# Kernel tuning notes

Measured on AMD Instinct MI355X. Metric: run time of the kernel, lower is better.

The kernel has to match this reference:

```python
import jax, jax.numpy as jnp
import numpy as np

N_NODES = 1_000_000
N_EDGES = 32_000_000

def setup_inputs() -> dict:
    key = jax.random.key(0)
    ks = jax.random.split(key, 7)
    x = jax.random.normal(ks[0], (N_NODES, 1), dtype=jnp.float32)
    edge_index = jax.random.randint(ks[1], (2, N_EDGES), 0, N_NODES, dtype=jnp.int32)
    W1 = jax.random.normal(ks[2], (1, 4), dtype=jnp.float32)
    b1 = jax.random.normal(ks[3], (4,), dtype=jnp.float32)
    W2 = jax.random.normal(ks[4], (4, 1), dtype=jnp.float32)
    b2 = jax.random.normal(ks[5], (1,), dtype=jnp.float32)
    Wsage = jax.random.normal(ks[6], (1, 1), dtype=jnp.float32)
    return {"x": x, "edge_index": edge_index, "W1": W1, "b1": b1,
            "W2": W2, "b2": b2, "Wsage": Wsage}

def reference(x, edge_index, W1, b1, W2, b2, Wsage):
    # MLP: Linear(1,4) -> ReLU -> Linear(4,1)
    h = jax.nn.relu(x @ W1 + b1) @ W2 + b2  # [N,1]
    # SAGEConv(1,1, root_weight=False, bias=False): mean-aggregate neighbors, then linear
    src, dst = edge_index[0], edge_index[1]
    n = h.shape[0]
    msgs = jnp.take(h, src, axis=0)                       # [E,1] gather
    summed = jax.ops.segment_sum(msgs, dst, num_segments=n)  # [N,1]
    cnt = jax.ops.segment_sum(jnp.ones((msgs.shape[0], 1), h.dtype), dst, num_segments=n)
    mean = summed / jnp.maximum(cnt, 1.0)                 # isolated nodes -> 0
    return mean @ Wsage
```

## Files before the change

kernel.cpp:

```cpp
#include <hip/hip_runtime.h>

__global__ void node_mlp_kernel(const float* __restrict__ x,
                                const float* __restrict__ W1,
                                const float* __restrict__ b1,
                                const float* __restrict__ W2,
                                const float* __restrict__ b2,
                                float* __restrict__ h, int N) {
    const float w10 = W1[0], w11 = W1[1], w12 = W1[2], w13 = W1[3];
    const float b10 = b1[0], b11 = b1[1], b12 = b1[2], b13 = b1[3];
    const float w20 = W2[0], w21 = W2[1], w22 = W2[2], w23 = W2[3];
    const float b2v = b2[0];
    int i = blockIdx.x * blockDim.x + threadIdx.x;
    if (i < N) {
        float xv = x[i];
        float acc = b2v;
        acc += fmaxf(fmaf(xv, w10, b10), 0.0f) * w20;
        acc += fmaxf(fmaf(xv, w11, b11), 0.0f) * w21;
        acc += fmaxf(fmaf(xv, w12, b12), 0.0f) * w22;
        acc += fmaxf(fmaf(xv, w13, b13), 0.0f) * w23;
        h[i] = acc;
    }
}

#define NBINS    256
#define NSUB     8
#define BIN_CAP  131072
#define SUBCAP   (BIN_CAP / NSUB)
#define CHUNK    4096
#define BLK      256
#define EPT      16
#define MAGIC_SH 42
#define PBITS    12
#define VBITS    17
#define VBIAS    (1 << (VBITS - 1))
#define VMAX     (VBIAS - 1)

__global__ void init_cursor_kernel(int* __restrict__ cursor) {
    int t = blockIdx.x * blockDim.x + threadIdx.x;
    if (t < NBINS * NSUB) cursor[t] = (t >> 3) * BIN_CAP + (t & (NSUB - 1)) * SUBCAP;
}

__device__ __forceinline__ int bin_of(int d, unsigned long long magic) {
    return (int)(((unsigned long long)(unsigned)d * magic) >> MAGIC_SH);
}

__global__ __launch_bounds__(BLK, 4)
void bin_scatter_kernel(const int* __restrict__ src,
                        const int* __restrict__ dst,
                        const float* __restrict__ h,
                        int* __restrict__ cursor,
                        unsigned* __restrict__ binned, int E,
                        int DIV, unsigned long long magic) {
    __shared__ int  lhist[NBINS];
    __shared__ int  lbase[NBINS];
    __shared__ int  gbase[NBINS];
    __shared__ int2 stage[CHUNK];

    const int t = threadIdx.x;
    lhist[t] = 0;
    __syncthreads();

    const int e0 = blockIdx.x * CHUNK;
    const int e1 = min(E, e0 + CHUNK);
    const int nval = e1 - e0;
    const int k = blockIdx.x & (NSUB - 1);

    int pk[EPT];
    int rk[EPT];
    #pragma unroll
    for (int it = 0; it < EPT / 4; ++it) {
        int e = e0 + 4 * (t + it * BLK);
        int4 d;
        if (e + 3 < e1) {
            d = *(const int4*)(dst + e);
        } else {
            d.x = (e + 0 < e1) ? dst[e + 0] : -1;
            d.y = (e + 1 < e1) ? dst[e + 1] : -1;
            d.z = (e + 2 < e1) ? dst[e + 2] : -1;
            d.w = (e + 3 < e1) ? dst[e + 3] : -1;
        }
        #pragma unroll
        for (int j = 0; j < 4; ++j) {
            int dd = (j == 0) ? d.x : (j == 1) ? d.y : (j == 2) ? d.z : d.w;
            int p = -1, r = 0;
            if (dd >= 0) {
                int b = bin_of(dd, magic);
                p = (b << PBITS) | (dd - b * DIV);
                r = atomicAdd(&lhist[b], 1);
            }
            pk[4 * it + j] = p;
            rk[4 * it + j] = r;
        }
    }
    __syncthreads();

    if (t < 64) {
        const int b4 = t * 4;
        int v[4]; int s = 0;
        #pragma unroll
        for (int j = 0; j < 4; ++j) { v[j] = lhist[b4 + j]; s += v[j]; }
        int inc = s;
        #pragma unroll
        for (int dlt = 1; dlt < 64; dlt <<= 1) {
            int u = __shfl_up(inc, dlt, 64);
            if (t >= dlt) inc += u;
        }
        int excl = inc - s;
        #pragma unroll
        for (int j = 0; j < 4; ++j) {
            lbase[b4 + j] = excl; excl += v[j];
        }
    }
    __syncthreads();

    int r0 = atomicAdd(&cursor[t * NSUB + k], lhist[t]);

    #pragma unroll
    for (int it = 0; it < EPT / 4; ++it) {
        int e = e0 + 4 * (t + it * BLK);
        int4 s4 = make_int4(0, 0, 0, 0);
        if (e + 3 < e1) {
            s4 = *(const int4*)(src + e);
        } else {
            if (e + 0 < e1) s4.x = src[e + 0];
            if (e + 1 < e1) s4.y = src[e + 1];
            if (e + 2 < e1) s4.z = src[e + 2];
            if (e + 3 < e1) s4.w = src[e + 3];
        }
        #pragma unroll
        for (int j = 0; j < 4; ++j) {
            int p = pk[4 * it + j];
            if (p >= 0) {
                int ss = (j == 0) ? s4.x : (j == 1) ? s4.y : (j == 2) ? s4.z : s4.w;
                int fx = __float2int_rn(h[ss] * 256.0f);
                fx = min(max(fx, -VMAX), VMAX) + VBIAS;
                int slot = lbase[p >> PBITS] + rk[4 * it + j];
                stage[slot] = make_int2(p, fx);
            }
        }
    }
    gbase[t] = r0;
    __syncthreads();

    const int subend_off = (k + 1) * SUBCAP;
    for (int i = t; i < nval; i += BLK) {
        int2 ent = stage[i];
        int b = ent.x >> PBITS;
        int addr = gbase[b] + (i - lbase[b]);
        if (addr < b * BIN_CAP + subend_off)
            binned[addr] = ((unsigned)(ent.x & ((1 << PBITS) - 1)) << VBITS)
                           | (unsigned)ent.y;
    }
}

#define RBLK 1024

__global__ __launch_bounds__(RBLK)
void bin_reduce_kernel(const unsigned* __restrict__ binned,
                       const int* __restrict__ cursor,
                       const float* __restrict__ Wsage,
                       float* __restrict__ out, int N, int DIV) {
    extern __shared__ unsigned acc32[];
    const int b = blockIdx.x;
    const int t = threadIdx.x;
    for (int i = t; i < DIV; i += RBLK) acc32[i] = 0u;
    __syncthreads();

    const unsigned vmask = (1u << VBITS) - 1;
    #pragma unroll 1
    for (int k = 0; k < NSUB; ++k) {
        const int sub_base = b * BIN_CAP + k * SUBCAP;
        int count = cursor[b * NSUB + k] - sub_base;
        if (count > SUBCAP) count = SUBCAP;
        const uint4* sub4 = (const uint4*)(binned + sub_base);
        const int nquad = count >> 2;
        for (int i = t; i < nquad; i += RBLK) {
            uint4 p = sub4[i];
            atomicAdd(&acc32[p.x >> VBITS], (1u << 24) + (p.x & vmask));
            atomicAdd(&acc32[p.y >> VBITS], (1u << 24) + (p.y & vmask));
            atomicAdd(&acc32[p.z >> VBITS], (1u << 24) + (p.z & vmask));
            atomicAdd(&acc32[p.w >> VBITS], (1u << 24) + (p.w & vmask));
        }
        int tail = count & 3;
        if (t < tail) {
            unsigned e = binned[sub_base + (nquad << 2) + t];
            atomicAdd(&acc32[e >> VBITS], (1u << 24) + (e & vmask));
        }
    }
    __syncthreads();

    const float ws = Wsage[0];
    const int n0 = b * DIV;
    for (int i = t; i < DIV; i += RBLK) {
        int n = n0 + i;
        if (n < N) {
            unsigned T = acc32[i];
            unsigned cnt = T >> 24;
            int sfx = (int)(T & 0xFFFFFFu) - (int)(cnt << 16);
            float sum = (float)sfx * (1.0f / 256.0f);
            float c   = (float)cnt;
            out[n] = (sum / fmaxf(c, 1.0f)) * ws;
        }
    }
}

#define PACK_C 4294967296.0

__global__ void edge_scatter_kernel(const int* __restrict__ src,
                                    const int* __restrict__ dst,
                                    const float* __restrict__ h,
                                    double* __restrict__ acc, int E) {
    int tid = blockIdx.x * blockDim.x + threadIdx.x;
    int nthreads = gridDim.x * blockDim.x;
    int E4 = E >> 2;
    const int4* src4 = (const int4*)src;
    const int4* dst4 = (const int4*)dst;
    for (int i = tid; i < E4; i += nthreads) {
        int4 s = src4[i];
        int4 d = dst4[i];
        unsafeAtomicAdd(&acc[d.x], (double)h[s.x] + PACK_C);
        unsafeAtomicAdd(&acc[d.y], (double)h[s.y] + PACK_C);
        unsafeAtomicAdd(&acc[d.z], (double)h[s.z] + PACK_C);
        unsafeAtomicAdd(&acc[d.w], (double)h[s.w] + PACK_C);
    }
    for (int e = (E4 << 2) + tid; e < E; e += nthreads)
        unsafeAtomicAdd(&acc[dst[e]], (double)h[src[e]] + PACK_C);
}

__global__ void finalize_kernel(const double* __restrict__ acc,
                                const float* __restrict__ Wsage,
                                float* __restrict__ out, int N) {
    const float ws = Wsage[0];
    int i = blockIdx.x * blockDim.x + threadIdx.x;
    if (i < N) {
        double t = acc[i];
        double cd = floor(t * (1.0 / PACK_C) + 0.5);
        double sd = t - cd * PACK_C;
        out[i] = (float)(sd / (double)fmaxf((float)cd, 1.0f)) * ws;
    }
}

extern "C" void kernel_launch(void* const* d_in, const int* in_sizes, int n_in,
                              void* d_out, int out_size, void* d_ws, size_t ws_size,
                              hipStream_t stream) {
    const float* x     = (const float*)d_in[0];
    const int*   edge  = (const int*)d_in[1];
    const float* W1    = (const float*)d_in[2];
    const float* b1    = (const float*)d_in[3];
    const float* W2    = (const float*)d_in[4];
    const float* b2    = (const float*)d_in[5];
    const float* Wsage = (const float*)d_in[6];

    const int N = in_sizes[0];
    const int E = in_sizes[1] / 2;
    const int* src = edge;
    const int* dst = edge + E;

    const int DIV = (N + NBINS - 1) / NBINS;
    const unsigned long long magic =
        ((1ULL << MAGIC_SH) + (unsigned long long)DIV - 1) / (unsigned long long)DIV;

    size_t off_h      = 0;
    size_t off_cursor = off_h + (size_t)N * sizeof(float);
    size_t off_binned = (off_cursor + (size_t)NBINS * NSUB * sizeof(int) + 255) & ~(size_t)255;
    size_t need = off_binned + (size_t)NBINS * BIN_CAP * sizeof(unsigned);

    float* h = (float*)((char*)d_ws + off_h);

    node_mlp_kernel<<<(N + BLK - 1) / BLK, BLK, 0, stream>>>(x, W1, b1, W2, b2, h, N);

    if (ws_size >= need && DIV < (1 << PBITS)) {
        int*      cursor = (int*)((char*)d_ws + off_cursor);
        unsigned* binned = (unsigned*)((char*)d_ws + off_binned);

        init_cursor_kernel<<<(NBINS * NSUB + BLK - 1) / BLK, BLK, 0, stream>>>(cursor);

        int nchunks = (E + CHUNK - 1) / CHUNK;
        bin_scatter_kernel<<<nchunks, BLK, 0, stream>>>(src, dst, h, cursor, binned, E,
                                                        DIV, magic);

        size_t lds_bytes = (size_t)DIV * sizeof(unsigned);
        bin_reduce_kernel<<<NBINS, RBLK, lds_bytes, stream>>>(binned, cursor,
                                                              Wsage, (float*)d_out,
                                                              N, DIV);
    } else {
        double* acc = (double*)((char*)d_ws + ((off_cursor + 7) & ~(size_t)7));
        hipMemsetAsync(acc, 0, (size_t)N * sizeof(double), stream);
        edge_scatter_kernel<<<2048, BLK, 0, stream>>>(src, dst, h, acc, E);
        finalize_kernel<<<(N + BLK - 1) / BLK, BLK, 0, stream>>>(acc, Wsage, (float*)d_out, N);
    }
}
```

Baseline: 341.5 us.

## Shrink scatter LDS staging, hoist src/h gathers before histogram, raise occupancy

The bin scatter kernel now loads src together with dst in the first pass and issues the h[src] gathers early, so their latency overlaps the histogram and scan phases. The per-edge rank is packed into the payload register instead of a separate array. The shared staging buffer shrinks from int2 to a 32-bit payload plus a byte bin id, and launch bounds are raised from 4 to 6 blocks per CU. The risks are extra register pressure from holding the gathered h values across the scan, and reliance on rank and bin fitting into the packed bit fields.

```diff
diff --git a/kernel.cpp b/kernel.cpp
--- a/kernel.cpp
+++ b/kernel.cpp
@@ -44,17 +44,18 @@
     return (int)(((unsigned long long)(unsigned)d * magic) >> MAGIC_SH);
 }
 
-__global__ __launch_bounds__(BLK, 4)
+__global__ __launch_bounds__(BLK, 6)
 void bin_scatter_kernel(const int* __restrict__ src,
                         const int* __restrict__ dst,
                         const float* __restrict__ h,
                         int* __restrict__ cursor,
                         unsigned* __restrict__ binned, int E,
                         int DIV, unsigned long long magic) {
-    __shared__ int  lhist[NBINS];
-    __shared__ int  lbase[NBINS];
-    __shared__ int  gbase[NBINS];
-    __shared__ int2 stage[CHUNK];
+    __shared__ int           lhist[NBINS];
+    __shared__ int           lbase[NBINS];
+    __shared__ int           gbase[NBINS];
+    __shared__ unsigned      stageP[CHUNK];
+    __shared__ unsigned char binsU8[CHUNK];
 
     const int t = threadIdx.x;
     lhist[t] = 0;
@@ -65,31 +66,36 @@
     const int nval = e1 - e0;
     const int k = blockIdx.x & (NSUB - 1);
 
-    int pk[EPT];
-    int rk[EPT];
+    unsigned pk[EPT];
+    float    hv[EPT];
     #pragma unroll
     for (int it = 0; it < EPT / 4; ++it) {
         int e = e0 + 4 * (t + it * BLK);
-        int4 d;
+        int4 d, s4;
         if (e + 3 < e1) {
-            d = *(const int4*)(dst + e);
+            d  = *(const int4*)(dst + e);
+            s4 = *(const int4*)(src + e);
         } else {
-            d.x = (e + 0 < e1) ? dst[e + 0] : -1;
-            d.y = (e + 1 < e1) ? dst[e + 1] : -1;
-            d.z = (e + 2 < e1) ? dst[e + 2] : -1;
-            d.w = (e + 3 < e1) ? dst[e + 3] : -1;
+            d.x = (e + 0 < e1) ? dst[e + 0] : 0;
+            d.y = (e + 1 < e1) ? dst[e + 1] : 0;
+            d.z = (e + 2 < e1) ? dst[e + 2] : 0;
+            d.w = (e + 3 < e1) ? dst[e + 3] : 0;
+            s4.x = (e + 0 < e1) ? src[e + 0] : 0;
+            s4.y = (e + 1 < e1) ? src[e + 1] : 0;
+            s4.z = (e + 2 < e1) ? src[e + 2] : 0;
+            s4.w = (e + 3 < e1) ? src[e + 3] : 0;
         }
         #pragma unroll
         for (int j = 0; j < 4; ++j) {
-            int dd = (j == 0) ? d.x : (j == 1) ? d.y : (j == 2) ? d.z : d.w;
-            int p = -1, r = 0;
-            if (dd >= 0) {
+            if (e + j < e1) {
+                int dd = (j == 0) ? d.x : (j == 1) ? d.y : (j == 2) ? d.z : d.w;
+                int ss = (j == 0) ? s4.x : (j == 1) ? s4.y : (j == 2) ? s4.z : s4.w;
                 int b = bin_of(dd, magic);
-                p = (b << PBITS) | (dd - b * DIV);
-                r = atomicAdd(&lhist[b], 1);
+                int r = atomicAdd(&lhist[b], 1);
+                pk[4 * it + j] = ((unsigned)r << 20) | ((unsigned)b << PBITS)
+                                 | (unsigned)(dd - b * DIV);
+                hv[4 * it + j] = h[ss];
             }
-            pk[4 * it + j] = p;
-            rk[4 * it + j] = r;
         }
     }
     __syncthreads();
@@ -118,24 +124,16 @@
     #pragma unroll
     for (int it = 0; it < EPT / 4; ++it) {
         int e = e0 + 4 * (t + it * BLK);
-        int4 s4 = make_int4(0, 0, 0, 0);
-        if (e + 3 < e1) {
-            s4 = *(const int4*)(src + e);
-        } else {
-            if (e + 0 < e1) s4.x = src[e + 0];
-            if (e + 1 < e1) s4.y = src[e + 1];
-            if (e + 2 < e1) s4.z = src[e + 2];
-            if (e + 3 < e1) s4.w = src[e + 3];
-        }
         #pragma unroll
         for (int j = 0; j < 4; ++j) {
-            int p = pk[4 * it + j];
-            if (p >= 0) {
-                int ss = (j == 0) ? s4.x : (j == 1) ? s4.y : (j == 2) ? s4.z : s4.w;
-                int fx = __float2int_rn(h[ss] * 256.0f);
+            if (e + j < e1) {
+                unsigned p = pk[4 * it + j];
+                int fx = __float2int_rn(hv[4 * it + j] * 256.0f);
                 fx = min(max(fx, -VMAX), VMAX) + VBIAS;
-                int slot = lbase[p >> PBITS] + rk[4 * it + j];
-                stage[slot] = make_int2(p, fx);
+                unsigned b = (p >> PBITS) & 0xFFu;
+                int slot = lbase[b] + (int)(p >> 20);
+                stageP[slot] = ((p & 0xFFFu) << VBITS) | (unsigned)fx;
+                binsU8[slot] = (unsigned char)b;
             }
         }
     }
@@ -144,12 +142,11 @@
 
     const int subend_off = (k + 1) * SUBCAP;
     for (int i = t; i < nval; i += BLK) {
-        int2 ent = stage[i];
-        int b = ent.x >> PBITS;
+        unsigned pay = stageP[i];
+        int b = binsU8[i];
         int addr = gbase[b] + (i - lbase[b]);
         if (addr < b * BIN_CAP + subend_off)
-            binned[addr] = ((unsigned)(ent.x & ((1 << PBITS) - 1)) << VBITS)
-                           | (unsigned)ent.y;
+            binned[addr] = pay;
     }
 }
 
```

Result: faster. 314.4 us (-7.9%).
